# Kernel tuning notes

Hardware: AMD Instinct MI355X
Metric: run time of the kernel (lower is better)

## Reference

```python
import jax, jax.numpy as jnp
import numpy as np
from jax import lax

EPS = 1e-5

def silu(x):
    return x * jax.nn.sigmoid(x)

def setup_inputs() -> dict:
    key = jax.random.key(0)
    ks = jax.random.split(key, 8)
    B, T, H, W = 8, 32, 128, 128
    x = jax.random.normal(ks[0], (B, 1, T, H, W), jnp.float32)
    w_spatial = jax.random.normal(ks[1], (3, 1, 3, 3), jnp.float32) * 0.3
    b_spatial = jax.random.normal(ks[2], (3,), jnp.float32) * 0.1
    w_temporal = jax.random.normal(ks[3], (3, 1, 7, 1), jnp.float32) * 0.3
    b_temporal = jax.random.normal(ks[4], (3,), jnp.float32) * 0.1
    sn_weight = jnp.ones((1, 3, 1, 1, 1), jnp.float32)
    sn_bias = jnp.zeros((1, 3, 1, 1, 1), jnp.float32)
    mean_weight = jnp.ones((3,), jnp.float32)
    var_weight = jnp.ones((3,), jnp.float32)
    w_kv_s = jax.random.normal(ks[5], (2, T), jnp.float32) * (1.0 / np.sqrt(T))
    w_kv_t = jax.random.normal(ks[6], (2, H * W), jnp.float32) * (1.0 / np.sqrt(H * W))
    return dict(x=x, w_spatial=w_spatial, b_spatial=b_spatial,
                w_temporal=w_temporal, b_temporal=b_temporal,
                sn_weight=sn_weight, sn_bias=sn_bias,
                mean_weight=mean_weight, var_weight=var_weight,
                w_kv_s=w_kv_s, w_kv_t=w_kv_t)

def reference(x, w_spatial, b_spatial, w_temporal, b_temporal,
              sn_weight, sn_bias, mean_weight, var_weight, w_kv_s, w_kv_t):
    b, _, t, h, w = x.shape
    C = 3
    # --- spatial cone: timeIsHidden -> Conv2d(1,3,3,pad=1) -> SiLU ---
    xs = x.transpose(0, 2, 1, 3, 4).reshape(b * t, 1, h, w)  # (b t) c h w
    y = lax.conv_general_dilated(xs, w_spatial, (1, 1), ((1, 1), (1, 1)))
    y = silu(y + b_spatial[None, :, None, None])
    y = y.reshape(b, t, C, h, w).transpose(0, 2, 1, 3, 4)  # [b,3,t,h,w]
    # --- temporal cone: spaceIsHidden -> depthwise Conv2d(3,3,(7,1),groups=3) -> SiLU ---
    # kernel is (7,1) so convolving [b,3,t,hw] along t with width-1 in hw is identical math
    yt = y.reshape(b, C, t, h * w)
    z = lax.conv_general_dilated(yt, w_temporal, (1, 1), ((3, 3), (0, 0)),
                                 feature_group_count=C)
    z = silu(z + b_temporal[None, :, None, None]).reshape(b, C, t, h, w)
    # --- gain stage 1: SiLU + SwitchNorm3d(3) (training-mode statistics) ---
    g = silu(z)
    xr = g.reshape(b, C, -1)
    mean_in = xr.mean(-1, keepdims=True)              # [b,C,1] instance stats
    var_in = xr.var(-1, ddof=1, keepdims=True)        # torch .var is unbiased
    temp = var_in + mean_in ** 2
    mean_ln = mean_in.mean(1, keepdims=True)          # layer stats
    var_ln = temp.mean(1, keepdims=True) - mean_ln ** 2
    mean_bn = mean_in.mean(0, keepdims=True)          # batch stats
    var_bn = temp.mean(0, keepdims=True) - mean_bn ** 2
    mw = jax.nn.softmax(mean_weight)
    vw = jax.nn.softmax(var_weight)
    mean = mw[0] * mean_in + mw[1] * mean_ln + mw[2] * mean_bn
    var = vw[0] * var_in + vw[1] * var_ln + vw[2] * var_bn
    xn = ((xr - mean) / jnp.sqrt(var + EPS)).reshape(b, C, t, h, w)
    xn = xn * sn_weight + sn_bias
    # --- gain stage 2: GainControl (spatial/temporal kv via 1x1 convs) ---
    hw = h * w
    # to_kv_spatial: Conv2d(t,2,1,bias=False) over time-as-channel == contraction over t
    kv_s = jnp.einsum('bcthw,ot->bcohw', xn, w_kv_s)   # [b,C,2,h,w]
    ks_ = jax.nn.softmax(kv_s[:, :, 0].reshape(b, C, hw), axis=-1)[:, :, None, :]
    vs_ = kv_s[:, :, 1].reshape(b, C, hw)[:, :, None, :]
    # to_kv_temporal: Conv2d(hw,2,1,bias=False) over space-as-channel == contraction over hw
    xflat = xn.reshape(b, C, t, hw)
    kv_t = jnp.einsum('bcts,os->bcot', xflat, w_kv_t)  # [b,C,2,t]
    kt_ = jax.nn.softmax(kv_t[:, :, 0], axis=-1)[..., None]
    vt_ = kv_t[:, :, 1][..., None]
    out = jnp.sqrt(kt_ * ks_) * (vt_ * vs_)            # [b,C,t,hw]
    return out.reshape(b, C, t, h, w)
```

## Files before the change

kernel.cpp:

```cpp
#include <hip/hip_runtime.h>
#include <hip/hip_bf16.h>

#define Bn 8
#define Cn 3
#define Tn 32
#define Hn 128
#define Wn 128
#define HWn (Hn * Wn)
#define Nn (Tn * HWn)
#define EPSn 1e-5f
#define NQ 4

__device__ __forceinline__ float silu_f(float v) {
    return v * __builtin_amdgcn_rcpf(1.0f + __expf(-v));
}

template<int QTR>
__device__ __forceinline__ void k12_body(
    const float* __restrict__ x, const float* __restrict__ wsp,
    const float* __restrict__ bsp, const float* __restrict__ wtp,
    const float* __restrict__ btp, const float* __restrict__ wkt,
    const float* __restrict__ wks,
    float* __restrict__ raw0, float* __restrict__ raw1,
    float* __restrict__ pt0p, float* __restrict__ pt1p,
    float* __restrict__ ss0p, float* __restrict__ ss1p)
{
    constexpr int O0 = QTR * 8;
    constexpr int O1 = O0 + 8;
    constexpr int SLO = (O0 - 3 < 0) ? 0 : (O0 - 3);
    constexpr int SHI = (O1 + 2 > Tn - 1) ? (Tn - 1) : (O1 + 2);

    const int tid = threadIdx.x;
    const int lane = tid & 63;
    const int wave = tid >> 6;
    const int row = blockIdx.x * 4 + wave;
    const int bc  = blockIdx.y;
    const int b = bc / 3, c = bc % 3;
    const int col = lane * 2;

    float wsp_r[9], wt_r[7];
#pragma unroll
    for (int i = 0; i < 9; ++i) wsp_r[i] = wsp[c * 9 + i];
    const float bsp_r = bsp[c];
#pragma unroll
    for (int i = 0; i < 7; ++i) wt_r[i] = wtp[c * 7 + i];
    const float bt_r = btp[c];

    const float* xb = x + (size_t)b * Nn + (size_t)row * Wn + col;
    const bool upok = row > 0, dnok = row < Hn - 1;

    const float2 k0v = *(const float2*)(wkt + row * Wn + col);
    const float2 k1v = *(const float2*)(wkt + HWn + row * Wn + col);

    float2 ring[7];
    float2 a0 = make_float2(0.f, 0.f), a1 = make_float2(0.f, 0.f);
    float ps = 0.f, pq = 0.f;

#pragma unroll
    for (int tt = SLO; tt <= SHI + 3; ++tt) {
        if (tt <= SHI) {
            const float* xsl = xb + (size_t)tt * HWn;
            float2 xm = upok ? *(const float2*)(xsl - Wn) : make_float2(0.f, 0.f);
            float2 xc = *(const float2*)(xsl);
            float2 xp = dnok ? *(const float2*)(xsl + Wn) : make_float2(0.f, 0.f);
            float xv[3][4];
            {
                float lu, rd;
                lu = __shfl_up(xm.y, 1);  rd = __shfl_down(xm.x, 1);
                xv[0][0] = (lane == 0) ? 0.f : lu; xv[0][1] = xm.x; xv[0][2] = xm.y;
                xv[0][3] = (lane == 63) ? 0.f : rd;
                lu = __shfl_up(xc.y, 1);  rd = __shfl_down(xc.x, 1);
                xv[1][0] = (lane == 0) ? 0.f : lu; xv[1][1] = xc.x; xv[1][2] = xc.y;
                xv[1][3] = (lane == 63) ? 0.f : rd;
                lu = __shfl_up(xp.y, 1);  rd = __shfl_down(xp.x, 1);
                xv[2][0] = (lane == 0) ? 0.f : lu; xv[2][1] = xp.x; xv[2][2] = xp.y;
                xv[2][3] = (lane == 63) ? 0.f : rd;
            }
            float s0 = bsp_r, s1 = bsp_r;
#pragma unroll
            for (int i = 0; i < 3; ++i) {
#pragma unroll
                for (int j = 0; j < 3; ++j) {
                    const float wv = wsp_r[i * 3 + j];
                    s0 += wv * xv[i][j];
                    s1 += wv * xv[i][j + 1];
                }
            }
            ring[tt % 7].x = silu_f(s0);
            ring[tt % 7].y = silu_f(s1);
        }
        const int to = tt - 3;
        if (to >= O0 && to < O1) {
            float t0 = bt_r, t1 = bt_r;
#pragma unroll
            for (int k = 0; k < 7; ++k) {
                const int ts = to + k - 3;
                if (ts >= 0 && ts < Tn) {
                    const float wv = wt_r[k];
                    t0 += wv * ring[ts % 7].x;
                    t1 += wv * ring[ts % 7].y;
                }
            }
            const float g0 = silu_f(silu_f(t0));
            const float g1 = silu_f(silu_f(t1));
            const float wk0 = wks[to];
            const float wk1 = wks[Tn + to];
            a0.x += wk0 * g0; a0.y += wk0 * g1;
            a1.x += wk1 * g0; a1.y += wk1 * g1;
            ps += g0 + g1;
            pq += g0 * g0 + g1 * g1;
            float p0 = k0v.x * g0 + k0v.y * g1;
            float p1 = k1v.x * g0 + k1v.y * g1;
            p0 += __shfl_xor(p0, 1, 64); p0 += __shfl_xor(p0, 2, 64); p0 += __shfl_xor(p0, 4, 64);
            p1 += __shfl_xor(p1, 1, 64); p1 += __shfl_xor(p1, 2, 64); p1 += __shfl_xor(p1, 4, 64);
            float r = (lane & 1) ? p1 : p0;
            r += __shfl_xor(r, 8, 64);
            r += __shfl_xor(r, 16, 64);
            r += __shfl_xor(r, 32, 64);
            if (lane < 2) {
                float* dst = lane ? pt1p : pt0p;
                dst[((size_t)bc * Tn + to) * Hn + row] = r;
            }
        }
    }

    {
        float p0 = ps, p1 = pq;
        p0 += __shfl_xor(p0, 1, 64); p0 += __shfl_xor(p0, 2, 64); p0 += __shfl_xor(p0, 4, 64);
        p1 += __shfl_xor(p1, 1, 64); p1 += __shfl_xor(p1, 2, 64); p1 += __shfl_xor(p1, 4, 64);
        float r = (lane & 1) ? p1 : p0;
        r += __shfl_xor(r, 8, 64);
        r += __shfl_xor(r, 16, 64);
        r += __shfl_xor(r, 32, 64);
        if (lane == 0) ss0p[(size_t)bc * (Hn * NQ) + row * NQ + QTR] = r;
        if (lane == 1) ss1p[(size_t)bc * (Hn * NQ) + row * NQ + QTR] = r;
    }
    {
        const size_t off = (size_t)(QTR * 24 + bc) * HWn + (size_t)row * Wn + col;
        *(float2*)(raw0 + off) = a0;
        *(float2*)(raw1 + off) = a1;
    }
}

__global__ __launch_bounds__(256) void k12_conv(
    const float* __restrict__ x, const float* __restrict__ wsp,
    const float* __restrict__ bsp, const float* __restrict__ wtp,
    const float* __restrict__ btp, const float* __restrict__ wkt,
    const float* __restrict__ wks,
    float* __restrict__ raw0, float* __restrict__ raw1,
    float* __restrict__ pt0p, float* __restrict__ pt1p,
    float* __restrict__ ss0p, float* __restrict__ ss1p)
{
    switch (blockIdx.z) {
    case 0: k12_body<0>(x, wsp, bsp, wtp, btp, wkt, wks, raw0, raw1, pt0p, pt1p, ss0p, ss1p); break;
    case 1: k12_body<1>(x, wsp, bsp, wtp, btp, wkt, wks, raw0, raw1, pt0p, pt1p, ss0p, ss1p); break;
    case 2: k12_body<2>(x, wsp, bsp, wtp, btp, wkt, wks, raw0, raw1, pt0p, pt1p, ss0p, ss1p); break;
    default: k12_body<3>(x, wsp, bsp, wtp, btp, wkt, wks, raw0, raw1, pt0p, pt1p, ss0p, ss1p); break;
    }
}

__global__ __launch_bounds__(256) void k3a_reduce(
    const float* __restrict__ pt0p, const float* __restrict__ pt1p,
    const float* __restrict__ ss0p, const float* __restrict__ ss1p,
    const float* __restrict__ wkt, const float* __restrict__ wks,
    float* __restrict__ kvt0r, float* __restrict__ kvt1r,
    float* __restrict__ ssS, float* __restrict__ ssSS, float* __restrict__ wsum)
{
    const int blk = blockIdx.x;
    const int tid = threadIdx.x;
    if (blk < Bn * Cn) {
        const int t = tid >> 3, g = tid & 7;
        const float4* p0 = (const float4*)(pt0p + ((size_t)blk * Tn + t) * Hn) + g * 4;
        const float4* p1 = (const float4*)(pt1p + ((size_t)blk * Tn + t) * Hn) + g * 4;
        float4 A0 = p0[0], A1 = p0[1], A2 = p0[2], A3 = p0[3];
        float4 B0 = p1[0], B1 = p1[1], B2 = p1[2], B3 = p1[3];
        float s0 = ((A0.x + A0.y) + (A0.z + A0.w)) + ((A1.x + A1.y) + (A1.z + A1.w))
                 + ((A2.x + A2.y) + (A2.z + A2.w)) + ((A3.x + A3.y) + (A3.z + A3.w));
        float s1 = ((B0.x + B0.y) + (B0.z + B0.w)) + ((B1.x + B1.y) + (B1.z + B1.w))
                 + ((B2.x + B2.y) + (B2.z + B2.w)) + ((B3.x + B3.y) + (B3.z + B3.w));
        s0 += __shfl_xor(s0, 1, 64); s0 += __shfl_xor(s0, 2, 64); s0 += __shfl_xor(s0, 4, 64);
        s1 += __shfl_xor(s1, 1, 64); s1 += __shfl_xor(s1, 2, 64); s1 += __shfl_xor(s1, 4, 64);
        if (g == 0) { kvt0r[blk * Tn + t] = s0; kvt1r[blk * Tn + t] = s1; }
        const float4* q0 = (const float4*)(ss0p + (size_t)blk * (Hn * NQ));
        const float4* q1 = (const float4*)(ss1p + (size_t)blk * (Hn * NQ));
        float a = 0.f, bb = 0.f;
        if (tid < Hn * NQ / 4) {
            float4 a4 = q0[tid], b4 = q1[tid];
            a = (a4.x + a4.y) + (a4.z + a4.w);
            bb = (b4.x + b4.y) + (b4.z + b4.w);
        }
        __shared__ float r0[256], r1[256];
        r0[tid] = a; r1[tid] = bb;
        __syncthreads();
        for (int off = 128; off > 0; off >>= 1) {
            if (tid < off) { r0[tid] += r0[tid + off]; r1[tid] += r1[tid + off]; }
            __syncthreads();
        }
        if (tid == 0) { ssS[blk] = r0[0]; ssSS[blk] = r1[0]; }
    } else {
        const float4* w0 = (const float4*)wkt;
        const float4* w1 = (const float4*)(wkt + HWn);
        float l0 = 0.f, l1 = 0.f;
        for (int i = tid; i < HWn / 4; i += 256) {
            float4 t0 = w0[i], t1 = w1[i];
            l0 += (t0.x + t0.y) + (t0.z + t0.w);
            l1 += (t1.x + t1.y) + (t1.z + t1.w);
        }
        __shared__ float r0[256], r1[256];
        r0[tid] = l0; r1[tid] = l1;
        __syncthreads();
        for (int off = 128; off > 0; off >>= 1) {
            if (tid < off) { r0[tid] += r0[tid + off]; r1[tid] += r1[tid + off]; }
            __syncthreads();
        }
        if (tid == 0) { wsum[0] = r0[0]; wsum[1] = r1[0]; }
        if (tid < 64) {
            float v = wks[tid];
            v += __shfl_xor(v, 1, 64); v += __shfl_xor(v, 2, 64);
            v += __shfl_xor(v, 4, 64); v += __shfl_xor(v, 8, 64);
            v += __shfl_xor(v, 16, 64);
            if (tid == 0) wsum[2] = v;
            if (tid == 32) wsum[3] = v;
        }
    }
}

__global__ __launch_bounds__(256) void k3b_finalize(
    const float* __restrict__ kvt0r, const float* __restrict__ kvt1r,
    const float* __restrict__ ssS, const float* __restrict__ ssSS,
    const float* __restrict__ mean_w, const float* __restrict__ var_w,
    const float* __restrict__ snw, const float* __restrict__ snb,
    const float* __restrict__ wsum,
    float* __restrict__ scale, float* __restrict__ shift, float* __restrict__ A)
{
    const int tid = threadIdx.x;
    __shared__ float kvt0[Bn * Cn * Tn], kvt1[Bn * Cn * Tn];
    __shared__ float sW[4];
    for (int i = tid; i < Bn * Cn * Tn; i += 256) { kvt0[i] = kvt0r[i]; kvt1[i] = kvt1r[i]; }
    if (tid < 4) sW[tid] = wsum[tid];
    __shared__ float sh_mean[24], sh_var[24], sh_temp[24];
    __shared__ float sh_mln[8], sh_vln[8], sh_mbn[3], sh_vbn[3];
    __shared__ float sh_mw[3], sh_vw[3];
    __shared__ float sh_scale[24], sh_shift[24];
    if (tid < 24) {
        float S = ssS[tid], SS = ssSS[tid];
        const float Nf = (float)Nn;
        float mean = S / Nf;
        float var = (SS - S * mean) / (Nf - 1.0f);
        sh_mean[tid] = mean; sh_var[tid] = var; sh_temp[tid] = var + mean * mean;
    }
    __syncthreads();
    if (tid == 0) {
        for (int b = 0; b < Bn; ++b) {
            float m = 0.f, tp = 0.f;
            for (int c = 0; c < Cn; ++c) { m += sh_mean[b * 3 + c]; tp += sh_temp[b * 3 + c]; }
            m *= (1.0f / 3.0f); tp *= (1.0f / 3.0f);
            sh_mln[b] = m; sh_vln[b] = tp - m * m;
        }
        for (int c = 0; c < Cn; ++c) {
            float m = 0.f, tp = 0.f;
            for (int b = 0; b < Bn; ++b) { m += sh_mean[b * 3 + c]; tp += sh_temp[b * 3 + c]; }
            m *= 0.125f; tp *= 0.125f;
            sh_mbn[c] = m; sh_vbn[c] = tp - m * m;
        }
        {
            float m0 = mean_w[0], m1 = mean_w[1], m2 = mean_w[2];
            float mm = fmaxf(m0, fmaxf(m1, m2));
            float e0 = __expf(m0 - mm), e1 = __expf(m1 - mm), e2 = __expf(m2 - mm);
            float inv = 1.0f / (e0 + e1 + e2);
            sh_mw[0] = e0 * inv; sh_mw[1] = e1 * inv; sh_mw[2] = e2 * inv;
        }
        {
            float v0 = var_w[0], v1 = var_w[1], v2 = var_w[2];
            float vm = fmaxf(v0, fmaxf(v1, v2));
            float e0 = __expf(v0 - vm), e1 = __expf(v1 - vm), e2 = __expf(v2 - vm);
            float inv = 1.0f / (e0 + e1 + e2);
            sh_vw[0] = e0 * inv; sh_vw[1] = e1 * inv; sh_vw[2] = e2 * inv;
        }
    }
    __syncthreads();
    if (tid < 24) {
        int b = tid / 3, c = tid % 3;
        float mean = sh_mw[0] * sh_mean[tid] + sh_mw[1] * sh_mln[b] + sh_mw[2] * sh_mbn[c];
        float var  = sh_vw[0] * sh_var[tid]  + sh_vw[1] * sh_vln[b] + sh_vw[2] * sh_vbn[c];
        float inv = 1.0f / sqrtf(var + EPSn);
        float sc = inv * snw[c];
        float sf = snb[c] - mean * sc;
        sh_scale[tid] = sc; sh_shift[tid] = sf;
        scale[tid] = sc; shift[tid] = sf;
    }
    __syncthreads();
    for (int i = tid; i < Bn * Cn * Tn; i += 256) {
        int bc = i >> 5;
        kvt0[i] = sh_scale[bc] * kvt0[i] + sh_shift[bc] * sW[0];
        kvt1[i] = sh_scale[bc] * kvt1[i] + sh_shift[bc] * sW[1];
    }
    __syncthreads();
    if (tid < 24) {
        float m = -3.4e38f;
        for (int t = 0; t < Tn; ++t) m = fmaxf(m, kvt0[tid * Tn + t]);
        float se = 0.f;
        for (int t = 0; t < Tn; ++t) se += __expf(kvt0[tid * Tn + t] - m);
        float inv = 1.0f / se;
        for (int t = 0; t < Tn; ++t)
            A[tid * Tn + t] = sqrtf(__expf(kvt0[tid * Tn + t] - m) * inv) * kvt1[tid * Tn + t];
    }
}

__global__ __launch_bounds__(256) void k5a_maxsum(
    const float* __restrict__ raw0, const float* __restrict__ raw1,
    const float* __restrict__ scale, const float* __restrict__ shift,
    const float* __restrict__ wsum, float* __restrict__ v0s,
    float* __restrict__ v1s, float2* __restrict__ ms)
{
    const int ch = blockIdx.x;
    const int bc = blockIdx.y;
    const int tid = threadIdx.x, lane = tid & 63, wave = tid >> 6;
    const float sc = scale[bc], sf = shift[bc];
    const float c0 = sf * wsum[2], c1 = sf * wsum[3];
    const size_t idx = (size_t)bc * HWn + ch * 2048 + tid * 8;
    float4 r0a = make_float4(0.f, 0.f, 0.f, 0.f), r0b = r0a, r1a = r0a, r1b = r0a;
#pragma unroll
    for (int q = 0; q < NQ; ++q) {
        const float* p0 = raw0 + (size_t)q * 24 * HWn + idx;
        const float* p1 = raw1 + (size_t)q * 24 * HWn + idx;
        float4 t0 = ((const float4*)p0)[0], t1 = ((const float4*)p0)[1];
        float4 u0 = ((const float4*)p1)[0], u1 = ((const float4*)p1)[1];
        r0a.x += t0.x; r0a.y += t0.y; r0a.z += t0.z; r0a.w += t0.w;
        r0b.x += t1.x; r0b.y += t1.y; r0b.z += t1.z; r0b.w += t1.w;
        r1a.x += u0.x; r1a.y += u0.y; r1a.z += u0.z; r1a.w += u0.w;
        r1b.x += u1.x; r1b.y += u1.y; r1b.z += u1.z; r1b.w += u1.w;
    }
    float v0[8] = { sc * r0a.x + c0, sc * r0a.y + c0, sc * r0a.z + c0, sc * r0a.w + c0,
                    sc * r0b.x + c0, sc * r0b.y + c0, sc * r0b.z + c0, sc * r0b.w + c0 };
    float v1[8] = { sc * r1a.x + c1, sc * r1a.y + c1, sc * r1a.z + c1, sc * r1a.w + c1,
                    sc * r1b.x + c1, sc * r1b.y + c1, sc * r1b.z + c1, sc * r1b.w + c1 };
    ((float4*)(v0s + idx))[0] = make_float4(v0[0], v0[1], v0[2], v0[3]);
    ((float4*)(v0s + idx))[1] = make_float4(v0[4], v0[5], v0[6], v0[7]);
    ((float4*)(v1s + idx))[0] = make_float4(v1[0], v1[1], v1[2], v1[3]);
    ((float4*)(v1s + idx))[1] = make_float4(v1[4], v1[5], v1[6], v1[7]);
    float m = -3.4e38f;
#pragma unroll
    for (int i = 0; i < 8; ++i) m = fmaxf(m, v0[i]);
#pragma unroll
    for (int d = 1; d < 64; d <<= 1) m = fmaxf(m, __shfl_xor(m, d, 64));
    __shared__ float wm[4], wsm[4];
    if (lane == 0) wm[wave] = m;
    __syncthreads();
    const float M = fmaxf(fmaxf(wm[0], wm[1]), fmaxf(wm[2], wm[3]));
    float s = 0.f;
#pragma unroll
    for (int i = 0; i < 8; ++i) s += __expf(v0[i] - M);
#pragma unroll
    for (int d = 1; d < 64; d <<= 1) s += __shfl_xor(s, d, 64);
    if (lane == 0) wsm[wave] = s;
    __syncthreads();
    if (tid == 0) {
        float2 o; o.x = M; o.y = wsm[0] + wsm[1] + wsm[2] + wsm[3];
        ms[bc * 8 + ch] = o;
    }
}

__global__ __launch_bounds__(256) void k6_outer(
    const float* __restrict__ v0s, const float* __restrict__ v1s,
    const float2* __restrict__ ms, const float* __restrict__ A,
    float* __restrict__ out)
{
    const int ch = blockIdx.x;
    const int bc = blockIdx.y;
    const int tid = threadIdx.x;
    __shared__ float a[Tn];
    if (tid < Tn) a[tid] = A[bc * Tn + tid];
    float M = -3.4e38f;
#pragma unroll
    for (int j = 0; j < 8; ++j) M = fmaxf(M, ms[bc * 8 + j].x);
    float S = 0.f;
#pragma unroll
    for (int j = 0; j < 8; ++j) S += ms[bc * 8 + j].y * __expf(ms[bc * 8 + j].x - M);
    const float invS = __builtin_amdgcn_rcpf(S);
    const int s = ch * 1024 + tid * 4;
    float4 r0 = *(const float4*)(v0s + (size_t)bc * HWn + s);
    float4 r1 = *(const float4*)(v1s + (size_t)bc * HWn + s);
    float4 Bv;
    Bv.x = sqrtf(__expf(r0.x - M) * invS) * r1.x;
    Bv.y = sqrtf(__expf(r0.y - M) * invS) * r1.y;
    Bv.z = sqrtf(__expf(r0.z - M) * invS) * r1.z;
    Bv.w = sqrtf(__expf(r0.w - M) * invS) * r1.w;
    __syncthreads();
    float* op = out + (size_t)bc * Nn + s;
#pragma unroll
    for (int t = 0; t < Tn; ++t) {
        const float av = a[t];
        float4 o; o.x = av * Bv.x; o.y = av * Bv.y; o.z = av * Bv.z; o.w = av * Bv.w;
        *(float4*)(op + (size_t)t * HWn) = o;
    }
}

extern "C" void kernel_launch(void* const* d_in, const int* in_sizes, int n_in,
                              void* d_out, int out_size, void* d_ws, size_t ws_size,
                              hipStream_t stream) {
    const float* x          = (const float*)d_in[0];
    const float* w_spatial  = (const float*)d_in[1];
    const float* b_spatial  = (const float*)d_in[2];
    const float* w_temporal = (const float*)d_in[3];
    const float* b_temporal = (const float*)d_in[4];
    const float* sn_weight  = (const float*)d_in[5];
    const float* sn_bias    = (const float*)d_in[6];
    const float* mean_weight= (const float*)d_in[7];
    const float* var_weight = (const float*)d_in[8];
    const float* w_kv_s     = (const float*)d_in[9];
    const float* w_kv_t     = (const float*)d_in[10];
    float* out = (float*)d_out;
    float* ws  = (float*)d_ws;

    float* raw0  = ws;
    float* raw1  = raw0 + (size_t)NQ * Bn * Cn * HWn;
    float* pt0p  = raw1 + (size_t)NQ * Bn * Cn * HWn;
    float* pt1p  = pt0p + (size_t)Bn * Cn * Tn * Hn;
    float* ss0p  = pt1p + (size_t)Bn * Cn * Tn * Hn;
    float* ss1p  = ss0p + (size_t)Bn * Cn * Hn * NQ;
    float* v0s   = ss1p + (size_t)Bn * Cn * Hn * NQ;
    float* v1s   = v0s + (size_t)Bn * Cn * HWn;
    float* kvt0r = v1s + (size_t)Bn * Cn * HWn;
    float* kvt1r = kvt0r + Bn * Cn * Tn;
    float* ssS   = kvt1r + Bn * Cn * Tn;
    float* ssSS  = ssS + 24;
    float* scale = ssSS + 24;
    float* shift = scale + 24;
    float* A     = shift + 24;
    float* wsum  = A + Bn * Cn * Tn;
    float2* ms   = (float2*)(wsum + 4);

    k12_conv<<<dim3(Hn / 4, Bn * Cn, NQ), 256, 0, stream>>>(x, w_spatial, b_spatial,
                                                            w_temporal, b_temporal,
                                                            w_kv_t, w_kv_s,
                                                            raw0, raw1, pt0p, pt1p,
                                                            ss0p, ss1p);
    k3a_reduce<<<Bn * Cn + 1, 256, 0, stream>>>(pt0p, pt1p, ss0p, ss1p, w_kv_t, w_kv_s,
                                                kvt0r, kvt1r, ssS, ssSS, wsum);
    k3b_finalize<<<1, 256, 0, stream>>>(kvt0r, kvt1r, ssS, ssSS,
                                        mean_weight, var_weight, sn_weight, sn_bias,
                                        wsum, scale, shift, A);
    k5a_maxsum<<<dim3(8, Bn * Cn), 256, 0, stream>>>(raw0, raw1, scale, shift, wsum,
                                                     v0s, v1s, ms);
    k6_outer<<<dim3(16, Bn * Cn), 256, 0, stream>>>(v0s, v1s, ms, A, out);
}
```

Before: 66.20 us.

## Split fused conv into spatial kernel writing fp16 intermediate and temporal kernel

Splits the fused spatial+temporal convolution into a spatial-conv kernel, which computes all three channels from one x read and stores SiLU output as fp16, and a temporal-conv kernel that streams the fp16 intermediate. Time is now split into two chunks instead of four, so less halo work is recomputed and fewer partial buffers are written. This removes the redundant per-channel and per-quarter recomputation of the 3x3 conv and x reads. In exchange it adds a full round trip of a 25 MB fp16 tensor through memory and fp16 rounding of the intermediate, which may affect accuracy.

```diff
diff --git a/kernel.cpp b/kernel.cpp
--- a/kernel.cpp
+++ b/kernel.cpp
@@ -1,5 +1,6 @@
 #include <hip/hip_runtime.h>
 #include <hip/hip_bf16.h>
+#include <hip/hip_fp16.h>
 
 #define Bn 8
 #define Cn 3
@@ -9,48 +10,93 @@
 #define HWn (Hn * Wn)
 #define Nn (Tn * HWn)
 #define EPSn 1e-5f
-#define NQ 4
+#define QT 2
+#define SCH 128
+#define SSW (SCH * QT)
 
 __device__ __forceinline__ float silu_f(float v) {
     return v * __builtin_amdgcn_rcpf(1.0f + __expf(-v));
 }
 
-template<int QTR>
-__device__ __forceinline__ void k12_body(
+__global__ __launch_bounds__(256) void k1_spatial(
     const float* __restrict__ x, const float* __restrict__ wsp,
-    const float* __restrict__ bsp, const float* __restrict__ wtp,
+    const float* __restrict__ bsp, __half* __restrict__ y)
+{
+    const int tid = threadIdx.x, lane = tid & 63, wave = tid >> 6;
+    const int bt = blockIdx.x;
+    const int b = bt >> 5, t = bt & 31;
+    const int row = blockIdx.y * 4 + wave;
+    const int col = lane * 2;
+
+    float w[27], bb[3];
+#pragma unroll
+    for (int i = 0; i < 27; ++i) w[i] = wsp[i];
+#pragma unroll
+    for (int i = 0; i < 3; ++i) bb[i] = bsp[i];
+
+    const float* xsl = x + ((size_t)b * Tn + t) * HWn + (size_t)row * Wn + col;
+    const bool upok = row > 0, dnok = row < Hn - 1;
+    float2 xm = upok ? *(const float2*)(xsl - Wn) : make_float2(0.f, 0.f);
+    float2 xc = *(const float2*)(xsl);
+    float2 xp = dnok ? *(const float2*)(xsl + Wn) : make_float2(0.f, 0.f);
+    float xv[3][4];
+    {
+        float lu, rd;
+        lu = __shfl_up(xm.y, 1);  rd = __shfl_down(xm.x, 1);
+        xv[0][0] = (lane == 0) ? 0.f : lu; xv[0][1] = xm.x; xv[0][2] = xm.y;
+        xv[0][3] = (lane == 63) ? 0.f : rd;
+        lu = __shfl_up(xc.y, 1);  rd = __shfl_down(xc.x, 1);
+        xv[1][0] = (lane == 0) ? 0.f : lu; xv[1][1] = xc.x; xv[1][2] = xc.y;
+        xv[1][3] = (lane == 63) ? 0.f : rd;
+        lu = __shfl_up(xp.y, 1);  rd = __shfl_down(xp.x, 1);
+        xv[2][0] = (lane == 0) ? 0.f : lu; xv[2][1] = xp.x; xv[2][2] = xp.y;
+        xv[2][3] = (lane == 63) ? 0.f : rd;
+    }
+#pragma unroll
+    for (int c = 0; c < 3; ++c) {
+        float s0 = bb[c], s1 = bb[c];
+#pragma unroll
+        for (int i = 0; i < 3; ++i) {
+#pragma unroll
+            for (int j = 0; j < 3; ++j) {
+                const float wv = w[c * 9 + i * 3 + j];
+                s0 += wv * xv[i][j];
+                s1 += wv * xv[i][j + 1];
+            }
+        }
+        __half2 o = __floats2half2_rn(silu_f(s0), silu_f(s1));
+        *(__half2*)(y + ((size_t)(b * 3 + c) * Tn + t) * HWn + (size_t)row * Wn + col) = o;
+    }
+}
+
+template<int QTg>
+__device__ __forceinline__ void k2_body(
+    const __half* __restrict__ y, const float* __restrict__ wtp,
     const float* __restrict__ btp, const float* __restrict__ wkt,
     const float* __restrict__ wks,
     float* __restrict__ raw0, float* __restrict__ raw1,
     float* __restrict__ pt0p, float* __restrict__ pt1p,
     float* __restrict__ ss0p, float* __restrict__ ss1p)
 {
-    constexpr int O0 = QTR * 8;
-    constexpr int O1 = O0 + 8;
+    constexpr int O0 = QTg * 16;
+    constexpr int O1 = O0 + 16;
     constexpr int SLO = (O0 - 3 < 0) ? 0 : (O0 - 3);
     constexpr int SHI = (O1 + 2 > Tn - 1) ? (Tn - 1) : (O1 + 2);
 
-    const int tid = threadIdx.x;
-    const int lane = tid & 63;
-    const int wave = tid >> 6;
-    const int row = blockIdx.x * 4 + wave;
+    const int tid = threadIdx.x, lane = tid & 63, wave = tid >> 6;
+    const int sch = blockIdx.x * 2 + wave;
     const int bc  = blockIdx.y;
-    const int b = bc / 3, c = bc % 3;
-    const int col = lane * 2;
-
-    float wsp_r[9], wt_r[7];
-#pragma unroll
-    for (int i = 0; i < 9; ++i) wsp_r[i] = wsp[c * 9 + i];
-    const float bsp_r = bsp[c];
+    const int c = bc % 3;
+    const int s0i = sch * 128 + lane * 2;
+
+    float wt_r[7];
 #pragma unroll
     for (int i = 0; i < 7; ++i) wt_r[i] = wtp[c * 7 + i];
     const float bt_r = btp[c];
 
-    const float* xb = x + (size_t)b * Nn + (size_t)row * Wn + col;
-    const bool upok = row > 0, dnok = row < Hn - 1;
-
-    const float2 k0v = *(const float2*)(wkt + row * Wn + col);
-    const float2 k1v = *(const float2*)(wkt + HWn + row * Wn + col);
+    const __half* yb = y + (size_t)bc * Nn + s0i;
+    const float2 k0v = *(const float2*)(wkt + s0i);
+    const float2 k1v = *(const float2*)(wkt + HWn + s0i);
 
     float2 ring[7];
     float2 a0 = make_float2(0.f, 0.f), a1 = make_float2(0.f, 0.f);
@@ -59,35 +105,8 @@
 #pragma unroll
     for (int tt = SLO; tt <= SHI + 3; ++tt) {
         if (tt <= SHI) {
-            const float* xsl = xb + (size_t)tt * HWn;
-            float2 xm = upok ? *(const float2*)(xsl - Wn) : make_float2(0.f, 0.f);
-            float2 xc = *(const float2*)(xsl);
-            float2 xp = dnok ? *(const float2*)(xsl + Wn) : make_float2(0.f, 0.f);
-            float xv[3][4];
-            {
-                float lu, rd;
-                lu = __shfl_up(xm.y, 1);  rd = __shfl_down(xm.x, 1);
-                xv[0][0] = (lane == 0) ? 0.f : lu; xv[0][1] = xm.x; xv[0][2] = xm.y;
-                xv[0][3] = (lane == 63) ? 0.f : rd;
-                lu = __shfl_up(xc.y, 1);  rd = __shfl_down(xc.x, 1);
-                xv[1][0] = (lane == 0) ? 0.f : lu; xv[1][1] = xc.x; xv[1][2] = xc.y;
-                xv[1][3] = (lane == 63) ? 0.f : rd;
-                lu = __shfl_up(xp.y, 1);  rd = __shfl_down(xp.x, 1);
-                xv[2][0] = (lane == 0) ? 0.f : lu; xv[2][1] = xp.x; xv[2][2] = xp.y;
-                xv[2][3] = (lane == 63) ? 0.f : rd;
-            }
-            float s0 = bsp_r, s1 = bsp_r;
-#pragma unroll
-            for (int i = 0; i < 3; ++i) {
-#pragma unroll
-                for (int j = 0; j < 3; ++j) {
-                    const float wv = wsp_r[i * 3 + j];
-                    s0 += wv * xv[i][j];
-                    s1 += wv * xv[i][j + 1];
-                }
-            }
-            ring[tt % 7].x = silu_f(s0);
-            ring[tt % 7].y = silu_f(s1);
+            const __half2 hv = *(const __half2*)(yb + (size_t)tt * HWn);
+            ring[tt % 7] = __half22float2(hv);
         }
         const int to = tt - 3;
         if (to >= O0 && to < O1) {
@@ -119,7 +138,7 @@
             r += __shfl_xor(r, 32, 64);
             if (lane < 2) {
                 float* dst = lane ? pt1p : pt0p;
-                dst[((size_t)bc * Tn + to) * Hn + row] = r;
+                dst[((size_t)bc * Tn + to) * SCH + sch] = r;
             }
         }
     }
@@ -132,31 +151,28 @@
         r += __shfl_xor(r, 8, 64);
         r += __shfl_xor(r, 16, 64);
         r += __shfl_xor(r, 32, 64);
-        if (lane == 0) ss0p[(size_t)bc * (Hn * NQ) + row * NQ + QTR] = r;
-        if (lane == 1) ss1p[(size_t)bc * (Hn * NQ) + row * NQ + QTR] = r;
+        if (lane == 0) ss0p[(size_t)bc * SSW + sch * QT + QTg] = r;
+        if (lane == 1) ss1p[(size_t)bc * SSW + sch * QT + QTg] = r;
     }
     {
-        const size_t off = (size_t)(QTR * 24 + bc) * HWn + (size_t)row * Wn + col;
+        const size_t off = (size_t)(QTg * 24 + bc) * HWn + s0i;
         *(float2*)(raw0 + off) = a0;
         *(float2*)(raw1 + off) = a1;
     }
 }
 
-__global__ __launch_bounds__(256) void k12_conv(
-    const float* __restrict__ x, const float* __restrict__ wsp,
-    const float* __restrict__ bsp, const float* __restrict__ wtp,
+__global__ __launch_bounds__(128) void k2_temporal(
+    const __half* __restrict__ y, const float* __restrict__ wtp,
     const float* __restrict__ btp, const float* __restrict__ wkt,
     const float* __restrict__ wks,
     float* __restrict__ raw0, float* __restrict__ raw1,
     float* __restrict__ pt0p, float* __restrict__ pt1p,
     float* __restrict__ ss0p, float* __restrict__ ss1p)
 {
-    switch (blockIdx.z) {
-    case 0: k12_body<0>(x, wsp, bsp, wtp, btp, wkt, wks, raw0, raw1, pt0p, pt1p, ss0p, ss1p); break;
-    case 1: k12_body<1>(x, wsp, bsp, wtp, btp, wkt, wks, raw0, raw1, pt0p, pt1p, ss0p, ss1p); break;
-    case 2: k12_body<2>(x, wsp, bsp, wtp, btp, wkt, wks, raw0, raw1, pt0p, pt1p, ss0p, ss1p); break;
-    default: k12_body<3>(x, wsp, bsp, wtp, btp, wkt, wks, raw0, raw1, pt0p, pt1p, ss0p, ss1p); break;
-    }
+    if (blockIdx.z == 0)
+        k2_body<0>(y, wtp, btp, wkt, wks, raw0, raw1, pt0p, pt1p, ss0p, ss1p);
+    else
+        k2_body<1>(y, wtp, btp, wkt, wks, raw0, raw1, pt0p, pt1p, ss0p, ss1p);
 }
 
 __global__ __launch_bounds__(256) void k3a_reduce(
@@ -170,8 +186,8 @@
     const int tid = threadIdx.x;
     if (blk < Bn * Cn) {
         const int t = tid >> 3, g = tid & 7;
-        const float4* p0 = (const float4*)(pt0p + ((size_t)blk * Tn + t) * Hn) + g * 4;
-        const float4* p1 = (const float4*)(pt1p + ((size_t)blk * Tn + t) * Hn) + g * 4;
+        const float4* p0 = (const float4*)(pt0p + ((size_t)blk * Tn + t) * SCH) + g * 4;
+        const float4* p1 = (const float4*)(pt1p + ((size_t)blk * Tn + t) * SCH) + g * 4;
         float4 A0 = p0[0], A1 = p0[1], A2 = p0[2], A3 = p0[3];
         float4 B0 = p1[0], B1 = p1[1], B2 = p1[2], B3 = p1[3];
         float s0 = ((A0.x + A0.y) + (A0.z + A0.w)) + ((A1.x + A1.y) + (A1.z + A1.w))
@@ -181,10 +197,10 @@
         s0 += __shfl_xor(s0, 1, 64); s0 += __shfl_xor(s0, 2, 64); s0 += __shfl_xor(s0, 4, 64);
         s1 += __shfl_xor(s1, 1, 64); s1 += __shfl_xor(s1, 2, 64); s1 += __shfl_xor(s1, 4, 64);
         if (g == 0) { kvt0r[blk * Tn + t] = s0; kvt1r[blk * Tn + t] = s1; }
-        const float4* q0 = (const float4*)(ss0p + (size_t)blk * (Hn * NQ));
-        const float4* q1 = (const float4*)(ss1p + (size_t)blk * (Hn * NQ));
+        const float4* q0 = (const float4*)(ss0p + (size_t)blk * SSW);
+        const float4* q1 = (const float4*)(ss1p + (size_t)blk * SSW);
         float a = 0.f, bb = 0.f;
-        if (tid < Hn * NQ / 4) {
+        if (tid < SSW / 4) {
             float4 a4 = q0[tid], b4 = q1[tid];
             a = (a4.x + a4.y) + (a4.z + a4.w);
             bb = (b4.x + b4.y) + (b4.z + b4.w);
@@ -321,7 +337,7 @@
     const size_t idx = (size_t)bc * HWn + ch * 2048 + tid * 8;
     float4 r0a = make_float4(0.f, 0.f, 0.f, 0.f), r0b = r0a, r1a = r0a, r1b = r0a;
 #pragma unroll
-    for (int q = 0; q < NQ; ++q) {
+    for (int q = 0; q < QT; ++q) {
         const float* p0 = raw0 + (size_t)q * 24 * HWn + idx;
         const float* p1 = raw1 + (size_t)q * 24 * HWn + idx;
         float4 t0 = ((const float4*)p0)[0], t1 = ((const float4*)p0)[1];
@@ -413,13 +429,14 @@
     float* out = (float*)d_out;
     float* ws  = (float*)d_ws;
 
-    float* raw0  = ws;
-    float* raw1  = raw0 + (size_t)NQ * Bn * Cn * HWn;
-    float* pt0p  = raw1 + (size_t)NQ * Bn * Cn * HWn;
-    float* pt1p  = pt0p + (size_t)Bn * Cn * Tn * Hn;
-    float* ss0p  = pt1p + (size_t)Bn * Cn * Tn * Hn;
-    float* ss1p  = ss0p + (size_t)Bn * Cn * Hn * NQ;
-    float* v0s   = ss1p + (size_t)Bn * Cn * Hn * NQ;
+    __half* yh   = (__half*)ws;
+    float* raw0  = ws + 6291456;
+    float* raw1  = raw0 + (size_t)QT * Bn * Cn * HWn;
+    float* pt0p  = raw1 + (size_t)QT * Bn * Cn * HWn;
+    float* pt1p  = pt0p + (size_t)Bn * Cn * Tn * SCH;
+    float* ss0p  = pt1p + (size_t)Bn * Cn * Tn * SCH;
+    float* ss1p  = ss0p + (size_t)Bn * Cn * SSW;
+    float* v0s   = ss1p + (size_t)Bn * Cn * SSW;
     float* v1s   = v0s + (size_t)Bn * Cn * HWn;
     float* kvt0r = v1s + (size_t)Bn * Cn * HWn;
     float* kvt1r = kvt0r + Bn * Cn * Tn;
@@ -431,11 +448,11 @@
     float* wsum  = A + Bn * Cn * Tn;
     float2* ms   = (float2*)(wsum + 4);
 
-    k12_conv<<<dim3(Hn / 4, Bn * Cn, NQ), 256, 0, stream>>>(x, w_spatial, b_spatial,
-                                                            w_temporal, b_temporal,
-                                                            w_kv_t, w_kv_s,
-                                                            raw0, raw1, pt0p, pt1p,
-                                                            ss0p, ss1p);
+    k1_spatial<<<dim3(Bn * Tn, Hn / 4), 256, 0, stream>>>(x, w_spatial, b_spatial, yh);
+    k2_temporal<<<dim3(SCH / 2, Bn * Cn, QT), 128, 0, stream>>>(yh, w_temporal,
+                                                                b_temporal, w_kv_t,
+                                                                w_kv_s, raw0, raw1,
+                                                                pt0p, pt1p, ss0p, ss1p);
     k3a_reduce<<<Bn * Cn + 1, 256, 0, stream>>>(pt0p, pt1p, ss0p, ss1p, w_kv_t, w_kv_s,
                                                 kvt0r, kvt1r, ssS, ssSS, wsum);
     k3b_finalize<<<1, 256, 0, stream>>>(kvt0r, kvt1r, ssS, ssSS,
```

New measurement: 66.39 us. Within noise of the previous version (+0.3%).
